# Performance work log

Hardware: AMD Instinct MI355X
Metric: run time of the kernel (lower is better)

## Reference

```python
import jax, jax.numpy as jnp
import numpy as np

HEADS = 16
HEAD_DIM = 64  # dim // heads = 1024 // 16
SCALE = HEAD_DIM ** -0.5
NEG_INF = -1e30


def setup_inputs() -> dict:
    key = jax.random.key(0)
    ks = jax.random.split(key, 4)
    B, N, D = 4, 2048, 1024
    x = jax.random.normal(ks[0], (B, N, D), dtype=jnp.float32)
    pos_bias = jax.random.normal(ks[1], (HEADS, N, N), dtype=jnp.float32) * 0.02
    w_qkv = jax.random.normal(ks[2], (D, 3 * D), dtype=jnp.float32) * (D ** -0.5)
    w_proj = jax.random.normal(ks[3], (D, D), dtype=jnp.float32) * (D ** -0.5)
    b_proj = jnp.zeros((D,), dtype=jnp.float32)
    return {"x": x, "pos_bias": pos_bias, "w_qkv": w_qkv, "w_proj": w_proj, "b_proj": b_proj}


def reference(x, pos_bias, w_qkv, w_proj, b_proj):
    B, N, D = x.shape
    qkv = x @ w_qkv                                   # [B, N, 3D]
    q, k, v = jnp.split(qkv, 3, axis=-1)
    # '... n (h d) -> ... h n d'
    def to_heads(t):
        return t.reshape(B, N, HEADS, HEAD_DIM).transpose(0, 2, 1, 3)
    q, k, v = to_heads(q), to_heads(k), to_heads(v)
    q = q * SCALE
    sim = jnp.einsum('bhid,bhjd->bhij', q, k)         # [B, H, N, N]
    sim = sim + pos_bias                               # broadcast over batch
    causal = jnp.tril(jnp.ones((N, N), dtype=bool))
    sim = jnp.where(causal, sim, NEG_INF)
    attn = jax.nn.softmax(sim, axis=-1)
    out = jnp.einsum('bhij,bhjd->bhid', attn, v)      # [B, H, N, d]
    out = out.transpose(0, 2, 1, 3).reshape(B, N, HEADS * HEAD_DIM)
    return out @ w_proj + b_proj
```

## Files before the change

kernel.cpp:

```cpp
#include <hip/hip_runtime.h>
#include <hip/hip_bf16.h>
#include <math.h>

typedef __attribute__((ext_vector_type(8))) short bf16x8;
typedef __attribute__((ext_vector_type(4))) float f32x4;
typedef __attribute__((ext_vector_type(8))) unsigned short u16x8;

#define MFMA16(a, b, c) __builtin_amdgcn_mfma_f32_16x16x32_bf16(a, b, c, 0, 0, 0)
#define LOG2E 1.4426950408889634f

__device__ __forceinline__ unsigned short f2b(float f) {
  __hip_bfloat16 h = __float2bfloat16(f);
  return *reinterpret_cast<unsigned short*>(&h);
}

__device__ __forceinline__ unsigned int pk2(float lo, float hi) {
  return (unsigned int)f2b(lo) | ((unsigned int)f2b(hi) << 16);
}

__device__ __forceinline__ uint4 cvt8(const float* __restrict__ p) {
  float4 a = *(const float4*)p;
  float4 b = *(const float4*)(p + 4);
  union {
    unsigned short us[8];
    uint4 u;
  } r;
  r.us[0] = f2b(a.x); r.us[1] = f2b(a.y); r.us[2] = f2b(a.z); r.us[3] = f2b(a.w);
  r.us[4] = f2b(b.x); r.us[5] = f2b(b.y); r.us[6] = f2b(b.z); r.us[7] = f2b(b.w);
  return r.u;
}

__global__ __launch_bounds__(256) void conv_f32_bf16(
    const float* __restrict__ in, unsigned short* __restrict__ out) {
  size_t i = ((size_t)blockIdx.x * 256 + threadIdx.x) * 8;
  *(uint4*)&out[i] = cvt8(in + i);
}

__global__ __launch_bounds__(256) void transpose_f32_bf16(
    const float* __restrict__ in, unsigned short* __restrict__ out, int R,
    int C) {
  __shared__ unsigned short tile[64][72];
  const int tR = blockIdx.y * 64, tC = blockIdx.x * 64;
  const int t = threadIdx.x;
#pragma unroll
  for (int p = 0; p < 4; ++p) {
    int u = t + p * 256, r = u >> 4, c = (u & 15) * 4;
    float4 v = *(const float4*)&in[(size_t)(tR + r) * C + tC + c];
    tile[r][c] = f2b(v.x);
    tile[r][c + 1] = f2b(v.y);
    tile[r][c + 2] = f2b(v.z);
    tile[r][c + 3] = f2b(v.w);
  }
  __syncthreads();
#pragma unroll
  for (int p = 0; p < 2; ++p) {
    int u = t + p * 256, orow = u >> 3, oc = (u & 7) * 8;
    u16x8 v;
#pragma unroll
    for (int e = 0; e < 8; ++e) v[e] = tile[oc + e][orow];
    *(u16x8*)&out[(size_t)(tC + orow) * R + tR + oc] = v;
  }
}

template <int MODE>
__global__ __launch_bounds__(256, 2) void gemm_bt(
    const unsigned short* __restrict__ A, const unsigned short* __restrict__ Bt,
    unsigned short* __restrict__ O0, unsigned short* __restrict__ O1,
    unsigned short* __restrict__ O2, float* __restrict__ OF,
    const float* __restrict__ bias, int K, int N) {
  __shared__ unsigned short sA[128][40];
  __shared__ unsigned short sB[128][40];
  const int m0 = blockIdx.y * 128, n0 = blockIdx.x * 128;
  const int t = threadIdx.x;
  const int wave = t >> 6, lane = t & 63, quad = lane >> 4, t16 = lane & 15;
  const int wr = (wave >> 1) * 64, wc = (wave & 1) * 64;
  const int sr = t >> 2, sc = (t & 3) * 8;

  f32x4 acc[4][4];
#pragma unroll
  for (int i = 0; i < 4; ++i)
#pragma unroll
    for (int j = 0; j < 4; ++j) acc[i][j] = (f32x4){0.f, 0.f, 0.f, 0.f};

  const unsigned short* Ap = A + (size_t)(m0 + sr) * K + sc;
  const unsigned short* Bp = Bt + (size_t)(n0 + sr) * K + sc;
  const size_t rowK64 = (size_t)64 * K;

  for (int k0 = 0; k0 < K; k0 += 32) {
    uint4 a0 = *(const uint4*)(Ap + k0);
    uint4 a1 = *(const uint4*)(Ap + rowK64 + k0);
    uint4 b0 = *(const uint4*)(Bp + k0);
    uint4 b1 = *(const uint4*)(Bp + rowK64 + k0);
    __syncthreads();
    *(uint4*)&sA[sr][sc] = a0;
    *(uint4*)&sA[sr + 64][sc] = a1;
    *(uint4*)&sB[sr][sc] = b0;
    *(uint4*)&sB[sr + 64][sc] = b1;
    __syncthreads();
    bf16x8 af[4], bf[4];
#pragma unroll
    for (int i = 0; i < 4; ++i)
      af[i] = *(const bf16x8*)&sA[wr + i * 16 + t16][quad * 8];
#pragma unroll
    for (int j = 0; j < 4; ++j)
      bf[j] = *(const bf16x8*)&sB[wc + j * 16 + t16][quad * 8];
#pragma unroll
    for (int i = 0; i < 4; ++i)
#pragma unroll
      for (int j = 0; j < 4; ++j) acc[i][j] = MFMA16(af[i], bf[j], acc[i][j]);
  }

#pragma unroll
  for (int i = 0; i < 4; ++i) {
    const int mrow = m0 + wr + i * 16 + quad * 4;
#pragma unroll
    for (int j = 0; j < 4; ++j) {
      const int ncol = n0 + wc + j * 16 + t16;
#pragma unroll
      for (int r = 0; r < 4; ++r) {
        const float v = acc[i][j][r];
        const int mr = mrow + r;
        if (MODE == 0) {
          const int bb = mr >> 11, nn = mr & 2047;
          const int sec = ncol >> 10, rem = ncol & 1023;
          const int hh = rem >> 6, dd = rem & 63;
          const size_t bhh = (size_t)bb * 16 + hh;
          if (sec == 0)
            O0[(bhh * 2048 + nn) * 64 + dd] = f2b(v * (0.125f * LOG2E));
          else if (sec == 1)
            O1[(bhh * 2048 + nn) * 64 + dd] = f2b(v);
          else
            O2[(bhh * 64 + dd) * 2048 + nn] = f2b(v);
        } else {
          OF[(size_t)mr * N + ncol] = v + bias[ncol];
        }
      }
    }
  }
}

__global__ __launch_bounds__(256, 4) void attn_kernel(
    const unsigned short* __restrict__ Q, const unsigned short* __restrict__ Kb,
    const unsigned short* __restrict__ Vt, const float* __restrict__ PB,
    unsigned short* __restrict__ Ao) {
  __shared__ unsigned short sK[64][72];
  __shared__ unsigned short sV[64][72];
  __shared__ unsigned short sQP[64][72];

  const int bh = blockIdx.x & 63;
  const int qt = 31 - (blockIdx.x >> 6);
  const int h = bh & 15;
  const int b = bh >> 4;
  const int q0 = qt * 64;
  const int t = threadIdx.x;
  const int wave = t >> 6, lane = t & 63, quad = lane >> 4, t16 = lane & 15;
  const int kloc = quad * 4;

  const size_t qbase = ((size_t)bh * 2048 + q0) * 64;
#pragma unroll
  for (int p = 0; p < 2; ++p) {
    int u = t + p * 256, r = u >> 3, c = (u & 7) * 8;
    *(uint4*)&sQP[r][c] = *(const uint4*)&Q[qbase + r * 64 + c];
  }
  __syncthreads();
  const bf16x8 qa0 = *(const bf16x8*)&sQP[wave * 16 + t16][quad * 8];
  const bf16x8 qa1 = *(const bf16x8*)&sQP[wave * 16 + t16][32 + quad * 8];

  f32x4 accO[4];
#pragma unroll
  for (int i = 0; i < 4; ++i) accO[i] = (f32x4){0.f, 0.f, 0.f, 0.f};
  float m = -INFINITY, l = 0.f;

  const int qrow = q0 + wave * 16 + t16;
  const int r0 = t >> 3, c0 = (t & 7) * 8;
  const size_t kvrow = (size_t)bh * 2048 * 64;
  const float* pbp =
      PB + (size_t)h * 4194304 + (size_t)qrow * 2048 + kloc;

  uint4 kv0 = *(const uint4*)&Kb[kvrow + (size_t)r0 * 64 + c0];
  uint4 kv1 = *(const uint4*)&Kb[kvrow + (size_t)(r0 + 32) * 64 + c0];
  uint4 vv0 = *(const uint4*)&Vt[kvrow + (size_t)r0 * 2048 + c0];
  uint4 vv1 = *(const uint4*)&Vt[kvrow + (size_t)(r0 + 32) * 2048 + c0];
  f32x4 biasf[4];
#pragma unroll
  for (int fr = 0; fr < 4; ++fr)
    biasf[fr] = *(const f32x4*)&pbp[fr * 16];

  for (int kt = 0; kt <= qt; ++kt) {
    const int k0 = kt * 64;
    __syncthreads();
    *(uint4*)&sK[r0][c0] = kv0;
    *(uint4*)&sK[r0 + 32][c0] = kv1;
    *(uint4*)&sV[r0][c0] = vv0;
    *(uint4*)&sV[r0 + 32][c0] = vv1;
    __syncthreads();
    if (kt < qt) {
      const size_t nk = (size_t)(k0 + 64);
      kv0 = *(const uint4*)&Kb[kvrow + nk * 64 + (size_t)r0 * 64 + c0];
      kv1 = *(const uint4*)&Kb[kvrow + nk * 64 + (size_t)(r0 + 32) * 64 + c0];
      vv0 = *(const uint4*)&Vt[kvrow + nk + (size_t)r0 * 2048 + c0];
      vv1 = *(const uint4*)&Vt[kvrow + nk + (size_t)(r0 + 32) * 2048 + c0];
    }

    f32x4 s[4];
#pragma unroll
    for (int fr = 0; fr < 4; ++fr) {
      bf16x8 kb0 = *(const bf16x8*)&sK[fr * 16 + t16][quad * 8];
      bf16x8 kb1 = *(const bf16x8*)&sK[fr * 16 + t16][32 + quad * 8];
      f32x4 z = (f32x4){0.f, 0.f, 0.f, 0.f};
      z = MFMA16(kb0, qa0, z);
      z = MFMA16(kb1, qa1, z);
      s[fr] = z;
    }
#pragma unroll
    for (int fr = 0; fr < 4; ++fr)
#pragma unroll
      for (int r = 0; r < 4; ++r)
        s[fr][r] = fmaf(biasf[fr][r], LOG2E, s[fr][r]);
    if (kt == qt) {
#pragma unroll
      for (int fr = 0; fr < 4; ++fr)
#pragma unroll
        for (int r = 0; r < 4; ++r)
          if (k0 + fr * 16 + kloc + r > qrow) s[fr][r] = -1e30f;
    }
    if (kt < qt) {
#pragma unroll
      for (int fr = 0; fr < 4; ++fr)
        biasf[fr] = *(const f32x4*)&pbp[k0 + 64 + fr * 16];
    }

    float mxa = fmaxf(fmaxf(s[0][0], s[0][1]), fmaxf(s[0][2], s[0][3]));
    float mxb = fmaxf(fmaxf(s[1][0], s[1][1]), fmaxf(s[1][2], s[1][3]));
    float mxc = fmaxf(fmaxf(s[2][0], s[2][1]), fmaxf(s[2][2], s[2][3]));
    float mxd = fmaxf(fmaxf(s[3][0], s[3][1]), fmaxf(s[3][2], s[3][3]));
    float mx = fmaxf(fmaxf(mxa, mxb), fmaxf(mxc, mxd));
    mx = fmaxf(mx, __shfl_xor(mx, 16));
    mx = fmaxf(mx, __shfl_xor(mx, 32));

    float al = 1.f;
    const bool grow = __any(mx > m) != 0;
    if (grow) {
      const float mn = fmaxf(m, mx);
      al = exp2f(m - mn);
      m = mn;
    }
    float rsa = 0.f, rsb = 0.f;
#pragma unroll
    for (int fr = 0; fr < 4; ++fr) {
      float p0 = exp2f(s[fr][0] - m);
      float p1 = exp2f(s[fr][1] - m);
      float p2 = exp2f(s[fr][2] - m);
      float p3 = exp2f(s[fr][3] - m);
      s[fr][0] = p0; s[fr][1] = p1; s[fr][2] = p2; s[fr][3] = p3;
      rsa += p0 + p1;
      rsb += p2 + p3;
    }
    float rs = rsa + rsb;
    rs += __shfl_xor(rs, 16);
    rs += __shfl_xor(rs, 32);
    l = fmaf(l, al, rs);
    if (grow) {
#pragma unroll
      for (int r = 0; r < 4; ++r) {
        const float alr = __shfl(al, (lane & 48) + kloc + r);
        accO[0][r] *= alr;
        accO[1][r] *= alr;
        accO[2][r] *= alr;
        accO[3][r] *= alr;
      }
    }

#pragma unroll
    for (int fr = 0; fr < 4; ++fr) {
      uint2 pv;
      pv.x = pk2(s[fr][0], s[fr][1]);
      pv.y = pk2(s[fr][2], s[fr][3]);
      *(uint2*)&sQP[wave * 16 + t16][fr * 16 + kloc] = pv;
    }
    const bf16x8 pa0 = *(const bf16x8*)&sQP[wave * 16 + t16][quad * 8];
    const bf16x8 pa1 = *(const bf16x8*)&sQP[wave * 16 + t16][32 + quad * 8];
#pragma unroll
    for (int fc = 0; fc < 4; ++fc) {
      bf16x8 vb0 = *(const bf16x8*)&sV[fc * 16 + t16][quad * 8];
      bf16x8 vb1 = *(const bf16x8*)&sV[fc * 16 + t16][32 + quad * 8];
      accO[fc] = MFMA16(pa0, vb0, accO[fc]);
      accO[fc] = MFMA16(pa1, vb1, accO[fc]);
    }
  }

  const float inv = 1.f / l;
  float invr[4];
#pragma unroll
  for (int r = 0; r < 4; ++r) invr[r] = __shfl(inv, (lane & 48) + kloc + r);
  const size_t obase = (size_t)b * 2048 * 1024 + (size_t)h * 64;
#pragma unroll
  for (int fc = 0; fc < 4; ++fc)
#pragma unroll
    for (int r = 0; r < 4; ++r)
      Ao[obase + (size_t)(q0 + wave * 16 + quad * 4 + r) * 1024 + fc * 16 +
         t16] = f2b(accO[fc][r] * invr[r]);
}

extern "C" void kernel_launch(void* const* d_in, const int* in_sizes, int n_in,
                              void* d_out, int out_size, void* d_ws,
                              size_t ws_size, hipStream_t stream) {
  (void)in_sizes;
  (void)n_in;
  (void)out_size;
  (void)ws_size;
  const float* x = (const float*)d_in[0];
  const float* pb = (const float*)d_in[1];
  const float* wqkv = (const float*)d_in[2];
  const float* wpro = (const float*)d_in[3];
  const float* bpro = (const float*)d_in[4];

  unsigned short* ws = (unsigned short*)d_ws;
  unsigned short* wqkvT = ws;
  unsigned short* wproT = wqkvT + 3072 * 1024;
  unsigned short* Qb = wproT + 1024 * 1024;
  unsigned short* Kb = Qb + 8388608;
  unsigned short* Vtb = Kb + 8388608;
  unsigned short* Ao = Vtb + 8388608;
  unsigned short* xb = Ao;

  conv_f32_bf16<<<4096, 256, 0, stream>>>(x, xb);
  transpose_f32_bf16<<<dim3(48, 16), 256, 0, stream>>>(wqkv, wqkvT, 1024, 3072);
  transpose_f32_bf16<<<dim3(16, 16), 256, 0, stream>>>(wpro, wproT, 1024, 1024);
  gemm_bt<0><<<dim3(24, 64), 256, 0, stream>>>(xb, wqkvT, Qb, Kb, Vtb, nullptr,
                                               nullptr, 1024, 3072);
  attn_kernel<<<2048, 256, 0, stream>>>(Qb, Kb, Vtb, pb, Ao);
  gemm_bt<1><<<dim3(8, 64), 256, 0, stream>>>(Ao, wproT, nullptr, nullptr,
                                              nullptr, (float*)d_out, bpro,
                                              1024, 1024);
}
```

Baseline: 586.7 us.

## Load GEMM tiles directly into LDS with global_load_lds and raise occupancy

The bf16 GEMM now copies A and B tiles from global memory straight into LDS with the global_load_lds builtin, instead of going through registers. Each wave moves a contiguous 16-row strip, so the LDS padding has to go and the tiles become unpadded 128x32 arrays. The aim is to cut VGPR pressure and load/store instructions, and launch bounds are raised to allow three blocks per CU. The catch is that unpadded rows can cause LDS bank conflicts on the fragment reads, and correctness depends on the barrier waiting for the DMA loads to finish.

```diff
diff --git a/kernel.cpp b/kernel.cpp
--- a/kernel.cpp
+++ b/kernel.cpp
@@ -16,6 +16,13 @@
 
 __device__ __forceinline__ unsigned int pk2(float lo, float hi) {
   return (unsigned int)f2b(lo) | ((unsigned int)f2b(hi) << 16);
+}
+
+__device__ __forceinline__ void gload16(const unsigned short* g,
+                                        unsigned short* lds) {
+  __builtin_amdgcn_global_load_lds(
+      (const __attribute__((address_space(1))) unsigned int*)g,
+      (__attribute__((address_space(3))) unsigned int*)lds, 16, 0, 0);
 }
 
 __device__ __forceinline__ uint4 cvt8(const float* __restrict__ p) {
@@ -63,18 +70,17 @@
 }
 
 template <int MODE>
-__global__ __launch_bounds__(256, 2) void gemm_bt(
+__global__ __launch_bounds__(256, 3) void gemm_bt(
     const unsigned short* __restrict__ A, const unsigned short* __restrict__ Bt,
     unsigned short* __restrict__ O0, unsigned short* __restrict__ O1,
     unsigned short* __restrict__ O2, float* __restrict__ OF,
     const float* __restrict__ bias, int K, int N) {
-  __shared__ unsigned short sA[128][40];
-  __shared__ unsigned short sB[128][40];
+  __shared__ unsigned short sA[128][32];
+  __shared__ unsigned short sB[128][32];
   const int m0 = blockIdx.y * 128, n0 = blockIdx.x * 128;
   const int t = threadIdx.x;
   const int wave = t >> 6, lane = t & 63, quad = lane >> 4, t16 = lane & 15;
   const int wr = (wave >> 1) * 64, wc = (wave & 1) * 64;
-  const int sr = t >> 2, sc = (t & 3) * 8;
 
   f32x4 acc[4][4];
 #pragma unroll
@@ -82,20 +88,23 @@
 #pragma unroll
     for (int j = 0; j < 4; ++j) acc[i][j] = (f32x4){0.f, 0.f, 0.f, 0.f};
 
-  const unsigned short* Ap = A + (size_t)(m0 + sr) * K + sc;
-  const unsigned short* Bp = Bt + (size_t)(n0 + sr) * K + sc;
-  const size_t rowK64 = (size_t)64 * K;
+  const int srow = wave * 16 + (lane >> 2);
+  const int scol = (lane & 3) * 8;
+  const unsigned short* Ap0 = A + (size_t)(m0 + srow) * K + scol;
+  const unsigned short* Ap1 = A + (size_t)(m0 + srow + 64) * K + scol;
+  const unsigned short* Bp0 = Bt + (size_t)(n0 + srow) * K + scol;
+  const unsigned short* Bp1 = Bt + (size_t)(n0 + srow + 64) * K + scol;
+  unsigned short* ldsA0 = &sA[wave * 16][0];
+  unsigned short* ldsA1 = &sA[wave * 16 + 64][0];
+  unsigned short* ldsB0 = &sB[wave * 16][0];
+  unsigned short* ldsB1 = &sB[wave * 16 + 64][0];
 
   for (int k0 = 0; k0 < K; k0 += 32) {
-    uint4 a0 = *(const uint4*)(Ap + k0);
-    uint4 a1 = *(const uint4*)(Ap + rowK64 + k0);
-    uint4 b0 = *(const uint4*)(Bp + k0);
-    uint4 b1 = *(const uint4*)(Bp + rowK64 + k0);
     __syncthreads();
-    *(uint4*)&sA[sr][sc] = a0;
-    *(uint4*)&sA[sr + 64][sc] = a1;
-    *(uint4*)&sB[sr][sc] = b0;
-    *(uint4*)&sB[sr + 64][sc] = b1;
+    gload16(Ap0 + k0, ldsA0);
+    gload16(Ap1 + k0, ldsA1);
+    gload16(Bp0 + k0, ldsB0);
+    gload16(Bp1 + k0, ldsB1);
     __syncthreads();
     bf16x8 af[4], bf[4];
 #pragma unroll
```

After: 581.6 us. About the same (-0.9%).
